# Optimization experiments

Hardware: AMD Instinct MI355X
Metric: run time of the kernel (lower is better)

## Reference

```python
import jax, jax.numpy as jnp
import numpy as np

DPITCH_RANGE = 24.0
SCALE = 1.0

B, T, ND, SD, H = 8192, 256, 8, 3, 64
HIST = 64
L = T - HIST  # generated LSTM steps; L+1 outputs emitted
IN = ND + SD + 1


def setup_inputs() -> dict:
    key = jax.random.key(0)
    ks = jax.random.split(key, 11)
    s = 1.0 / np.sqrt(H)

    def u(k, shape):
        return jax.random.uniform(k, shape, jnp.float32, -s, s)

    return {
        "noise": jax.random.normal(ks[0], (B, T, ND), jnp.float32),
        "hist_x": jax.random.normal(ks[1], (B, HIST, SD), jnp.float32) * 0.1,
        "gap_duration": jax.random.uniform(ks[2], (B, L + 1, SD - 1), jnp.float32),
        "W_ih": u(ks[3], (4 * H, IN)),
        "W_hh": u(ks[4], (4 * H, H)),
        "b_ih": u(ks[5], (4 * H,)),
        "b_hh": u(ks[6], (4 * H,)),
        "W1": u(ks[7], (H, H)),
        "b1": u(ks[8], (H,)),
        "W2": u(ks[9], (1, H)),
        "b2": u(ks[10], (1,)),
    }


def reference(noise, hist_x, gap_duration, W_ih, W_hh, b_ih, b_hh, W1, b1, W2, b2):
    hist_len = hist_x.shape[1]
    bias = b_ih + b_hh

    def lstm_cell(x, h, c):
        # PyTorch gate order: i, f, g, o
        gates = x @ W_ih.T + h @ W_hh.T + bias
        i, f, g, o = jnp.split(gates, 4, axis=-1)
        c = jax.nn.sigmoid(f) * c + jax.nn.sigmoid(i) * jnp.tanh(g)
        h = jax.nn.sigmoid(o) * jnp.tanh(c)
        return h, c

    # ---- conditioning on history ----
    dist = jnp.cumsum(hist_x[:, :, -1:], axis=1)                 # [B,HIST,1]
    cond_in = jnp.concatenate([hist_x, dist, noise[:, :hist_len]], axis=-1)  # [B,HIST,IN]
    h0 = jnp.zeros((noise.shape[0], W_hh.shape[1]), noise.dtype)
    c0 = jnp.zeros_like(h0)

    def cond_step(carry, x_t):
        h, c = carry
        h, c = lstm_cell(x_t, h, c)
        return (h, c), None

    (h, c), _ = jax.lax.scan(cond_step, (h0, c0), jnp.swapaxes(cond_in, 0, 1))
    output = h                      # last LSTM output [B,H]
    dist = dist[:, -1, :]           # [B,1]

    gen_noise = noise[:, hist_len:]                               # [B,L,ND]
    # pad one zero step: the final LSTM update is computed but unused
    gen_noise = jnp.concatenate(
        [gen_noise, jnp.zeros((gen_noise.shape[0], 1, gen_noise.shape[2]), gen_noise.dtype)], axis=1)
    xs = (jnp.swapaxes(gap_duration, 0, 1), jnp.swapaxes(gen_noise, 0, 1))

    def gen_step(carry, x_t):
        h, c, out, dist = carry
        gd, nz = x_t
        z = jnp.tanh(jnp.tanh(out @ W1.T + b1) @ W2.T + b2)       # output_net
        dp = z * DPITCH_RANGE * SCALE                             # [B,1]
        x = jnp.concatenate([gd, dp], axis=-1)                    # [B,SD]
        dist = dist + dp
        inp = jnp.concatenate([x, dist, nz], axis=-1)             # [B,IN]
        h, c = lstm_cell(inp, h, c)
        return (h, c, h, dist), x

    _, gen_xs = jax.lax.scan(gen_step, (h, c, output, dist), xs)  # [L+1,B,SD]
    output_seq = jnp.swapaxes(gen_xs, 0, 1)                       # [B,L+1,SD]
    return jnp.concatenate([hist_x, output_seq], axis=1)          # [B,HIST+L+1,SD]
```

## Files before the change

kernel.cpp:

```cpp
#include <hip/hip_runtime.h>
#include <stdint.h>

typedef unsigned short u16;
typedef unsigned int u32;
typedef __attribute__((ext_vector_type(8))) short short8v;
typedef __attribute__((ext_vector_type(4))) float f32x4;

#define NB 16
#define HISTN 64
#define TGEN 193

#define S_NOISE 2048
#define S_HIST  192
#define S_GAP   386
#define S_OUT   771

#define HROW 104

__device__ __forceinline__ float b2f(u16 u) { return __uint_as_float(((u32)u) << 16); }
__device__ __forceinline__ u16 f2b(float f) {
    u32 u = __float_as_uint(f);
    u32 r = (u + 0x7fffu + ((u >> 16) & 1u)) >> 16;
    return (u16)r;
}
__device__ __forceinline__ float rcp_(float x) { return __builtin_amdgcn_rcpf(x); }
__device__ __forceinline__ float sigf(float x) { return rcp_(1.0f + __expf(-x)); }
__device__ __forceinline__ float tanhf_(float x) {
    return __builtin_fmaf(-2.0f, rcp_(1.0f + __expf(2.0f * x)), 1.0f);
}
__device__ __forceinline__ float ldv(const void* p, int idx, bool f32) {
    return f32 ? ((const float*)p)[idx] : b2f(((const u16*)p)[idx]);
}
__device__ __forceinline__ void sync_lds() {
    asm volatile("s_waitcnt lgkmcnt(0)" ::: "memory");
    __builtin_amdgcn_s_barrier();
}

extern "C" __global__ void __launch_bounds__(512, 4)
lstm_gen_kernel(const void* __restrict__ noise, const void* __restrict__ hist_x,
                const void* __restrict__ gap, const void* __restrict__ pW_ih,
                const void* __restrict__ pW_hh, const void* __restrict__ pb_ih,
                const void* __restrict__ pb_hh, const void* __restrict__ pW1,
                const void* __restrict__ pb1, const void* __restrict__ pW2,
                const void* __restrict__ pb2, void* __restrict__ out)
{
    __shared__ u16 hst[NB * HROW];
    __shared__ float zpl[NB * 20];

    const int tid = threadIdx.x;
    const int lane = tid & 63;
    const int w = tid >> 6;
    const int lg = lane >> 4;
    const int ln = lane & 15;

    bool is_f32 = false;
    {
        const u32* p = (const u32*)pW_hh;
        for (int i = 0; i < 64; i++) {
            u32 v = p[i];
            float a = b2f((u16)(v & 0xffffu));
            float bb = b2f((u16)(v >> 16));
            if (!(fabsf(a) <= 0.5f) || !(fabsf(bb) <= 0.5f)) is_f32 = true;
        }
    }

    for (int i = tid; i < NB * HROW / 2; i += 512) ((u32*)hst)[i] = 0u;

    short8v a00, a01, a02, a10, a11, a12;
#pragma unroll
    for (int T = 0; T < 2; T++) {
        const int j = (T << 5) | (w << 2) | (ln >> 2);
        const int g = ln & 3;
        const int row = (g << 6) | j;
        float wdp = ldv(pW_ih, row * 12 + 2, is_f32);
        u16 wdph = f2b(wdp);
        u16 wdpl = f2b(wdp - b2f(wdph));
        float wds = ldv(pW_ih, row * 12 + 3, is_f32);
        u16 wdsh = f2b(wds);
        u16 wdsl = f2b(wds - b2f(wdsh));
        short8v f0, f1, f2;
#pragma unroll
        for (int e = 0; e < 8; e++) {
            const int c = lg * 8 + e;
            f0[e] = (short)f2b(ldv(pW_hh, row * 64 + c, is_f32));
            f1[e] = (short)f2b(ldv(pW_hh, row * 64 + 32 + c, is_f32));
            u16 v = 0;
            if (c == 0 || c == 1) v = f2b(ldv(pW_ih, row * 12 + c, is_f32));
            else if (c == 2 || c == 3) v = wdph;
            else if (c == 4 || c == 5) v = wdsh;
            else if (c == 6) v = wdsl;
            else if (c == 7) v = wdpl;
            else if (c >= 8 && c < 16) v = f2b(ldv(pW_ih, row * 12 + (c - 4), is_f32));
            f2[e] = (short)v;
        }
        if (T == 0) { a00 = f0; a01 = f1; a02 = f2; }
        else        { a10 = f0; a11 = f1; a12 = f2; }
    }

    f32x4 bias0, bias1;
#pragma unroll
    for (int T = 0; T < 2; T++) {
        const int jc = (T << 5) | (w << 2) | lg;
        f32x4 bv;
#pragma unroll
        for (int q = 0; q < 4; q++) {
            const int row = (q << 6) | jc;
            bv[q] = ldv(pb_ih, row, is_f32) + ldv(pb_hh, row, is_f32);
        }
        if (T == 0) bias0 = bv; else bias1 = bv;
    }

    const bool mlpw = (w >= 4);
    short8v w1F0 = {}, w1F1 = {};
    f32x4 b1v = {0.f, 0.f, 0.f, 0.f};
    float w2L[4] = {0.f, 0.f, 0.f, 0.f};
    if (mlpw) {
        const int wp = w - 4;
        const int row1 = (wp << 4) | ln;
#pragma unroll
        for (int e = 0; e < 8; e++) {
            w1F0[e] = (short)f2b(ldv(pW1, row1 * 64 + lg * 8 + e, is_f32));
            w1F1[e] = (short)f2b(ldv(pW1, row1 * 64 + 32 + lg * 8 + e, is_f32));
        }
        const int rq = (wp << 4) | (lg << 2);
#pragma unroll
        for (int q = 0; q < 4; q++) {
            b1v[q] = ldv(pb1, rq + q, is_f32);
            w2L[q] = ldv(pW2, rq + q, is_f32);
        }
    }

    const bool owner = tid < NB;
    const size_t gb = (size_t)blockIdx.x * NB + (size_t)(tid & (NB - 1));
    const u16* nz_h = (const u16*)noise + gb * S_NOISE;
    const float* nz_f = (const float*)noise + gb * S_NOISE;
    const u16* hx_h = (const u16*)hist_x + gb * S_HIST;
    const float* hx_f = (const float*)hist_x + gb * S_HIST;
    const u16* gd_h = (const u16*)gap + gb * S_GAP;
    const float* gd_f = (const float*)gap + gb * S_GAP;
    u16* out_h = (u16*)out + gb * S_OUT;
    float* out_f = (float*)out + gb * S_OUT;

    float dist = 0.0f, b2v = 0.0f;
    float cv0 = 0.f, cv1 = 0.f, cv2 = 0.f;
    u32 n01 = 0, n23 = 0, n45 = 0, n67 = 0;

    auto ldnoise = [&](int t) {
        if (is_f32) {
            const float4* q = (const float4*)(nz_f + t * 8);
            float4 a = q[0], bq = q[1];
            n01 = (u32)f2b(a.x) | ((u32)f2b(a.y) << 16);
            n23 = (u32)f2b(a.z) | ((u32)f2b(a.w) << 16);
            n45 = (u32)f2b(bq.x) | ((u32)f2b(bq.y) << 16);
            n67 = (u32)f2b(bq.z) | ((u32)f2b(bq.w) << 16);
        } else {
            uint4 nv = *(const uint4*)(nz_h + t * 8);
            n01 = nv.x; n23 = nv.y; n45 = nv.z; n67 = nv.w;
        }
    };

    if (owner) {
        b2v = ldv(pb2, 0, is_f32);
        if (is_f32) { cv0 = hx_f[0]; cv1 = hx_f[1]; cv2 = hx_f[2]; }
        else { cv0 = b2f(hx_h[0]); cv1 = b2f(hx_h[1]); cv2 = b2f(hx_h[2]); }
        ldnoise(0);
    }

    float cst0 = 0.f, cst1 = 0.f;
    __syncthreads();

#pragma unroll 1
    for (int t = 0; t < HISTN; t++) {
        short8v bf0 = *(const short8v*)&hst[ln * HROW + lg * 8];
        short8v bf1 = *(const short8v*)&hst[ln * HROW + 32 + lg * 8];
        if (owner) {
            dist += cv2;
            u16 dph = f2b(cv2); u16 dpl = f2b(cv2 - b2f(dph));
            u16 dsh = f2b(dist); u16 dsl = f2b(dist - b2f(dsh));
            u16* hr = &hst[tid * HROW];
            *(u32*)&hr[64] = (u32)f2b(cv0) | ((u32)f2b(cv1) << 16);
            *(u32*)&hr[66] = (u32)dph | ((u32)dpl << 16);
            *(u32*)&hr[68] = (u32)dsh | ((u32)dsl << 16);
            *(u32*)&hr[70] = (u32)dsh | ((u32)dph << 16);
            *(u32*)&hr[72] = n01; *(u32*)&hr[74] = n23;
            *(u32*)&hr[76] = n45; *(u32*)&hr[78] = n67;
        }
        sync_lds();
        if (owner) {
            if (is_f32) { out_f[t*3] = cv0; out_f[t*3+1] = cv1; out_f[t*3+2] = cv2; }
            else { out_h[t*3] = f2b(cv0); out_h[t*3+1] = f2b(cv1); out_h[t*3+2] = f2b(cv2); }
            if (t + 1 < HISTN) {
                if (is_f32) { cv0 = hx_f[(t+1)*3]; cv1 = hx_f[(t+1)*3+1]; cv2 = hx_f[(t+1)*3+2]; }
                else { cv0 = b2f(hx_h[(t+1)*3]); cv1 = b2f(hx_h[(t+1)*3+1]); cv2 = b2f(hx_h[(t+1)*3+2]); }
                ldnoise(t + 1);
            } else {
                if (is_f32) { cv0 = gd_f[0]; cv1 = gd_f[1]; }
                else { u32 g = *(const u32*)gd_h; cv0 = b2f((u16)(g & 0xffffu)); cv1 = b2f((u16)(g >> 16)); }
                ldnoise(HISTN);
            }
        }
        short8v bf2 = *(const short8v*)&hst[ln * HROW + 64 + lg * 8];
        f32x4 acc0 = bias0, acc1 = bias1;
        acc0 = __builtin_amdgcn_mfma_f32_16x16x32_bf16(a00, bf0, acc0, 0, 0, 0);
        acc0 = __builtin_amdgcn_mfma_f32_16x16x32_bf16(a01, bf1, acc0, 0, 0, 0);
        acc0 = __builtin_amdgcn_mfma_f32_16x16x32_bf16(a02, bf2, acc0, 0, 0, 0);
        acc1 = __builtin_amdgcn_mfma_f32_16x16x32_bf16(a10, bf0, acc1, 0, 0, 0);
        acc1 = __builtin_amdgcn_mfma_f32_16x16x32_bf16(a11, bf1, acc1, 0, 0, 0);
        acc1 = __builtin_amdgcn_mfma_f32_16x16x32_bf16(a12, bf2, acc1, 0, 0, 0);
        float h0, h1;
        { float iv = sigf(acc0[0]), fv = sigf(acc0[1]), gv = tanhf_(acc0[2]), ov = sigf(acc0[3]);
          cst0 = fv * cst0 + iv * gv; h0 = ov * tanhf_(cst0); }
        { float iv = sigf(acc1[0]), fv = sigf(acc1[1]), gv = tanhf_(acc1[2]), ov = sigf(acc1[3]);
          cst1 = fv * cst1 + iv * gv; h1 = ov * tanhf_(cst1); }
        const int j0 = (w << 2) | lg;
        hst[ln * HROW + j0] = f2b(h0);
        hst[ln * HROW + j0 + 32] = f2b(h1);
        sync_lds();
    }

#pragma unroll 1
    for (int tg = 0; tg < TGEN; tg++) {
        short8v bf0 = *(const short8v*)&hst[ln * HROW + lg * 8];
        short8v bf1 = *(const short8v*)&hst[ln * HROW + 32 + lg * 8];
        if (mlpw) {
            f32x4 m0 = b1v;
            m0 = __builtin_amdgcn_mfma_f32_16x16x32_bf16(w1F0, bf0, m0, 0, 0, 0);
            m0 = __builtin_amdgcn_mfma_f32_16x16x32_bf16(w1F1, bf1, m0, 0, 0, 0);
            float p0 = w2L[0] * tanhf_(m0[0]) + w2L[1] * tanhf_(m0[1])
                     + w2L[2] * tanhf_(m0[2]) + w2L[3] * tanhf_(m0[3]);
            zpl[ln * 20 + (((w - 4) << 2) | lg)] = p0;
        }
        sync_lds();
        if (owner) {
            const float4* zr = (const float4*)&zpl[tid * 20];
            float4 z0 = zr[0], z1 = zr[1], z2 = zr[2], z3 = zr[3];
            float pre2 = b2v + z0.x + z0.y + z0.z + z0.w + z1.x + z1.y + z1.z + z1.w
                       + z2.x + z2.y + z2.z + z2.w + z3.x + z3.y + z3.z + z3.w;
            float zz = tanhf_(pre2);
            float dp = 24.0f * zz;
            dist += dp;
            u16 dph = f2b(dp); u16 dpl = f2b(dp - b2f(dph));
            u16 dsh = f2b(dist); u16 dsl = f2b(dist - b2f(dsh));
            u16* hr = &hst[tid * HROW];
            *(u32*)&hr[64] = (u32)f2b(cv0) | ((u32)f2b(cv1) << 16);
            *(u32*)&hr[66] = (u32)dph | ((u32)dpl << 16);
            *(u32*)&hr[68] = (u32)dsh | ((u32)dsl << 16);
            *(u32*)&hr[70] = (u32)dsh | ((u32)dph << 16);
            *(u32*)&hr[72] = n01; *(u32*)&hr[74] = n23;
            *(u32*)&hr[76] = n45; *(u32*)&hr[78] = n67;
            const int to = HISTN + tg;
            if (is_f32) { out_f[to*3] = cv0; out_f[to*3+1] = cv1; out_f[to*3+2] = dp; }
            else { out_h[to*3] = f2b(cv0); out_h[to*3+1] = f2b(cv1); out_h[to*3+2] = f2b(dp); }
        }
        sync_lds();
        if (owner && tg + 1 < TGEN) {
            if (is_f32) { cv0 = gd_f[(tg+1)*2]; cv1 = gd_f[(tg+1)*2+1]; }
            else { u32 g = *(const u32*)(gd_h + (tg+1)*2);
                   cv0 = b2f((u16)(g & 0xffffu)); cv1 = b2f((u16)(g >> 16)); }
            if (tg + 1 < TGEN - 1) ldnoise(HISTN + tg + 1);
            else { n01 = n23 = n45 = n67 = 0; }
        }
        short8v bf2 = *(const short8v*)&hst[ln * HROW + 64 + lg * 8];
        f32x4 acc0 = bias0, acc1 = bias1;
        acc0 = __builtin_amdgcn_mfma_f32_16x16x32_bf16(a00, bf0, acc0, 0, 0, 0);
        acc0 = __builtin_amdgcn_mfma_f32_16x16x32_bf16(a01, bf1, acc0, 0, 0, 0);
        acc0 = __builtin_amdgcn_mfma_f32_16x16x32_bf16(a02, bf2, acc0, 0, 0, 0);
        acc1 = __builtin_amdgcn_mfma_f32_16x16x32_bf16(a10, bf0, acc1, 0, 0, 0);
        acc1 = __builtin_amdgcn_mfma_f32_16x16x32_bf16(a11, bf1, acc1, 0, 0, 0);
        acc1 = __builtin_amdgcn_mfma_f32_16x16x32_bf16(a12, bf2, acc1, 0, 0, 0);
        float h0, h1;
        { float iv = sigf(acc0[0]), fv = sigf(acc0[1]), gv = tanhf_(acc0[2]), ov = sigf(acc0[3]);
          cst0 = fv * cst0 + iv * gv; h0 = ov * tanhf_(cst0); }
        { float iv = sigf(acc1[0]), fv = sigf(acc1[1]), gv = tanhf_(acc1[2]), ov = sigf(acc1[3]);
          cst1 = fv * cst1 + iv * gv; h1 = ov * tanhf_(cst1); }
        const int j0 = (w << 2) | lg;
        hst[ln * HROW + j0] = f2b(h0);
        hst[ln * HROW + j0 + 32] = f2b(h1);
        sync_lds();
    }
}

extern "C" void kernel_launch(void* const* d_in, const int* in_sizes, int n_in,
                              void* d_out, int out_size, void* d_ws, size_t ws_size,
                              hipStream_t stream) {
    (void)in_sizes; (void)n_in; (void)d_ws; (void)ws_size; (void)out_size;
    lstm_gen_kernel<<<512, 512, 0, stream>>>(
        d_in[0], d_in[1], d_in[2], d_in[3], d_in[4], d_in[5],
        d_in[6], d_in[7], d_in[8], d_in[9], d_in[10], d_out);
}
```

Measured before the change: 500.6 us.

## Double-buffer hidden state and apply dist/dp terms in fp32 to cut barriers

```diff
diff --git a/kernel.cpp b/kernel.cpp
--- a/kernel.cpp
+++ b/kernel.cpp
@@ -44,8 +44,9 @@
                 const void* __restrict__ pb1, const void* __restrict__ pW2,
                 const void* __restrict__ pb2, void* __restrict__ out)
 {
-    __shared__ u16 hst[NB * HROW];
-    __shared__ float zpl[NB * 20];
+    __shared__ u16 hst[2][NB * HROW];
+    __shared__ float hxl[HISTN][NB][3];
+    __shared__ float zpl[NB * 4];
 
     const int tid = threadIdx.x;
     const int lane = tid & 63;
@@ -64,7 +65,11 @@
         }
     }
 
-    for (int i = tid; i < NB * HROW / 2; i += 512) ((u32*)hst)[i] = 0u;
+    for (int i = tid; i < NB * HROW; i += 512) ((u32*)hst)[i] = 0u;
+    for (int i = tid; i < HISTN * NB * 3; i += 512) {
+        int t = i / 48, r = i % 48, b = r / 3, k = r % 3;
+        hxl[t][b][k] = ldv(hist_x, ((size_t)blockIdx.x * NB + b) * S_HIST + t * 3 + k, is_f32);
+    }
 
     short8v a00, a01, a02, a10, a11, a12;
 #pragma unroll
@@ -72,12 +77,6 @@
         const int j = (T << 5) | (w << 2) | (ln >> 2);
         const int g = ln & 3;
         const int row = (g << 6) | j;
-        float wdp = ldv(pW_ih, row * 12 + 2, is_f32);
-        u16 wdph = f2b(wdp);
-        u16 wdpl = f2b(wdp - b2f(wdph));
-        float wds = ldv(pW_ih, row * 12 + 3, is_f32);
-        u16 wdsh = f2b(wds);
-        u16 wdsl = f2b(wds - b2f(wdsh));
         short8v f0, f1, f2;
 #pragma unroll
         for (int e = 0; e < 8; e++) {
@@ -86,10 +85,6 @@
             f1[e] = (short)f2b(ldv(pW_hh, row * 64 + 32 + c, is_f32));
             u16 v = 0;
             if (c == 0 || c == 1) v = f2b(ldv(pW_ih, row * 12 + c, is_f32));
-            else if (c == 2 || c == 3) v = wdph;
-            else if (c == 4 || c == 5) v = wdsh;
-            else if (c == 6) v = wdsl;
-            else if (c == 7) v = wdpl;
             else if (c >= 8 && c < 16) v = f2b(ldv(pW_ih, row * 12 + (c - 4), is_f32));
             f2[e] = (short)v;
         }
@@ -97,17 +92,20 @@
         else        { a10 = f0; a11 = f1; a12 = f2; }
     }
 
-    f32x4 bias0, bias1;
+    f32x4 bias0, bias1, wd0, wd1, ws0, ws1;
 #pragma unroll
     for (int T = 0; T < 2; T++) {
         const int jc = (T << 5) | (w << 2) | lg;
-        f32x4 bv;
+        f32x4 bv, dv, sv;
 #pragma unroll
         for (int q = 0; q < 4; q++) {
             const int row = (q << 6) | jc;
             bv[q] = ldv(pb_ih, row, is_f32) + ldv(pb_hh, row, is_f32);
-        }
-        if (T == 0) bias0 = bv; else bias1 = bv;
+            dv[q] = ldv(pW_ih, row * 12 + 2, is_f32);
+            sv[q] = ldv(pW_ih, row * 12 + 3, is_f32);
+        }
+        if (T == 0) { bias0 = bv; wd0 = dv; ws0 = sv; }
+        else        { bias1 = bv; wd1 = dv; ws1 = sv; }
     }
 
     const bool mlpw = (w >= 4);
@@ -130,19 +128,19 @@
         }
     }
 
-    const bool owner = tid < NB;
-    const size_t gb = (size_t)blockIdx.x * NB + (size_t)(tid & (NB - 1));
+    const float b2v = ldv(pb2, 0, is_f32);
+
+    const size_t gb = (size_t)blockIdx.x * NB + (size_t)ln;
     const u16* nz_h = (const u16*)noise + gb * S_NOISE;
     const float* nz_f = (const float*)noise + gb * S_NOISE;
-    const u16* hx_h = (const u16*)hist_x + gb * S_HIST;
-    const float* hx_f = (const float*)hist_x + gb * S_HIST;
     const u16* gd_h = (const u16*)gap + gb * S_GAP;
     const float* gd_f = (const float*)gap + gb * S_GAP;
     u16* out_h = (u16*)out + gb * S_OUT;
     float* out_f = (float*)out + gb * S_OUT;
-
-    float dist = 0.0f, b2v = 0.0f;
-    float cv0 = 0.f, cv1 = 0.f, cv2 = 0.f;
+    const bool writer = (tid < NB);
+
+    float dist = 0.0f;
+    float cv0 = 0.f, cv1 = 0.f;
     u32 n01 = 0, n23 = 0, n45 = 0, n67 = 0;
 
     auto ldnoise = [&](int t) {
@@ -158,48 +156,39 @@
             n01 = nv.x; n23 = nv.y; n45 = nv.z; n67 = nv.w;
         }
     };
-
-    if (owner) {
-        b2v = ldv(pb2, 0, is_f32);
-        if (is_f32) { cv0 = hx_f[0]; cv1 = hx_f[1]; cv2 = hx_f[2]; }
-        else { cv0 = b2f(hx_h[0]); cv1 = b2f(hx_h[1]); cv2 = b2f(hx_h[2]); }
-        ldnoise(0);
-    }
-
+    auto ldgd = [&](int tg) {
+        if (is_f32) { cv0 = gd_f[tg * 2]; cv1 = gd_f[tg * 2 + 1]; }
+        else { u32 g = *(const u32*)(gd_h + tg * 2);
+               cv0 = b2f((u16)(g & 0xffffu)); cv1 = b2f((u16)(g >> 16)); }
+    };
+    auto mkbf2 = [&](float xa, float xb) {
+        short8v z = {};
+        if (lg == 0) { z[0] = (short)f2b(xa); z[1] = (short)f2b(xb); }
+        else if (lg == 1) {
+            z[0] = (short)(n01 & 0xffffu); z[1] = (short)(n01 >> 16);
+            z[2] = (short)(n23 & 0xffffu); z[3] = (short)(n23 >> 16);
+            z[4] = (short)(n45 & 0xffffu); z[5] = (short)(n45 >> 16);
+            z[6] = (short)(n67 & 0xffffu); z[7] = (short)(n67 >> 16);
+        }
+        return z;
+    };
+
+    if (lg == 1) ldnoise(0);
     float cst0 = 0.f, cst1 = 0.f;
+    int pc = 0;
     __syncthreads();
 
 #pragma unroll 1
     for (int t = 0; t < HISTN; t++) {
-        short8v bf0 = *(const short8v*)&hst[ln * HROW + lg * 8];
-        short8v bf1 = *(const short8v*)&hst[ln * HROW + 32 + lg * 8];
-        if (owner) {
-            dist += cv2;
-            u16 dph = f2b(cv2); u16 dpl = f2b(cv2 - b2f(dph));
-            u16 dsh = f2b(dist); u16 dsl = f2b(dist - b2f(dsh));
-            u16* hr = &hst[tid * HROW];
-            *(u32*)&hr[64] = (u32)f2b(cv0) | ((u32)f2b(cv1) << 16);
-            *(u32*)&hr[66] = (u32)dph | ((u32)dpl << 16);
-            *(u32*)&hr[68] = (u32)dsh | ((u32)dsl << 16);
-            *(u32*)&hr[70] = (u32)dsh | ((u32)dph << 16);
-            *(u32*)&hr[72] = n01; *(u32*)&hr[74] = n23;
-            *(u32*)&hr[76] = n45; *(u32*)&hr[78] = n67;
-        }
-        sync_lds();
-        if (owner) {
-            if (is_f32) { out_f[t*3] = cv0; out_f[t*3+1] = cv1; out_f[t*3+2] = cv2; }
-            else { out_h[t*3] = f2b(cv0); out_h[t*3+1] = f2b(cv1); out_h[t*3+2] = f2b(cv2); }
-            if (t + 1 < HISTN) {
-                if (is_f32) { cv0 = hx_f[(t+1)*3]; cv1 = hx_f[(t+1)*3+1]; cv2 = hx_f[(t+1)*3+2]; }
-                else { cv0 = b2f(hx_h[(t+1)*3]); cv1 = b2f(hx_h[(t+1)*3+1]); cv2 = b2f(hx_h[(t+1)*3+2]); }
-                ldnoise(t + 1);
-            } else {
-                if (is_f32) { cv0 = gd_f[0]; cv1 = gd_f[1]; }
-                else { u32 g = *(const u32*)gd_h; cv0 = b2f((u16)(g & 0xffffu)); cv1 = b2f((u16)(g >> 16)); }
-                ldnoise(HISTN);
-            }
-        }
-        short8v bf2 = *(const short8v*)&hst[ln * HROW + 64 + lg * 8];
+        const u16* hc = hst[pc];
+        u16* hn = hst[pc ^ 1];
+        short8v bf0 = *(const short8v*)&hc[ln * HROW + lg * 8];
+        short8v bf1 = *(const short8v*)&hc[ln * HROW + 32 + lg * 8];
+        float x2 = hxl[t][ln][2];
+        float x0f = 0.f, x1f = 0.f;
+        if (lg == 0) { x0f = hxl[t][ln][0]; x1f = hxl[t][ln][1]; }
+        dist += x2;
+        short8v bf2 = mkbf2(x0f, x1f);
         f32x4 acc0 = bias0, acc1 = bias1;
         acc0 = __builtin_amdgcn_mfma_f32_16x16x32_bf16(a00, bf0, acc0, 0, 0, 0);
         acc0 = __builtin_amdgcn_mfma_f32_16x16x32_bf16(a01, bf1, acc0, 0, 0, 0);
@@ -207,60 +196,36 @@
         acc1 = __builtin_amdgcn_mfma_f32_16x16x32_bf16(a10, bf0, acc1, 0, 0, 0);
         acc1 = __builtin_amdgcn_mfma_f32_16x16x32_bf16(a11, bf1, acc1, 0, 0, 0);
         acc1 = __builtin_amdgcn_mfma_f32_16x16x32_bf16(a12, bf2, acc1, 0, 0, 0);
+#pragma unroll
+        for (int q = 0; q < 4; q++) {
+            acc0[q] += wd0[q] * x2 + ws0[q] * dist;
+            acc1[q] += wd1[q] * x2 + ws1[q] * dist;
+        }
         float h0, h1;
         { float iv = sigf(acc0[0]), fv = sigf(acc0[1]), gv = tanhf_(acc0[2]), ov = sigf(acc0[3]);
           cst0 = fv * cst0 + iv * gv; h0 = ov * tanhf_(cst0); }
         { float iv = sigf(acc1[0]), fv = sigf(acc1[1]), gv = tanhf_(acc1[2]), ov = sigf(acc1[3]);
           cst1 = fv * cst1 + iv * gv; h1 = ov * tanhf_(cst1); }
         const int j0 = (w << 2) | lg;
-        hst[ln * HROW + j0] = f2b(h0);
-        hst[ln * HROW + j0 + 32] = f2b(h1);
+        hn[ln * HROW + j0] = f2b(h0);
+        hn[ln * HROW + j0 + 32] = f2b(h1);
+        if (writer) {
+            if (is_f32) { out_f[t*3] = x0f; out_f[t*3+1] = x1f; out_f[t*3+2] = x2; }
+            else { out_h[t*3] = f2b(x0f); out_h[t*3+1] = f2b(x1f); out_h[t*3+2] = f2b(x2); }
+        }
+        if (lg == 1) ldnoise(t + 1 < HISTN ? t + 1 : HISTN);
+        if (lg == 0 && t == HISTN - 1) ldgd(0);
         sync_lds();
+        pc ^= 1;
     }
 
 #pragma unroll 1
     for (int tg = 0; tg < TGEN; tg++) {
-        short8v bf0 = *(const short8v*)&hst[ln * HROW + lg * 8];
-        short8v bf1 = *(const short8v*)&hst[ln * HROW + 32 + lg * 8];
-        if (mlpw) {
-            f32x4 m0 = b1v;
-            m0 = __builtin_amdgcn_mfma_f32_16x16x32_bf16(w1F0, bf0, m0, 0, 0, 0);
-            m0 = __builtin_amdgcn_mfma_f32_16x16x32_bf16(w1F1, bf1, m0, 0, 0, 0);
-            float p0 = w2L[0] * tanhf_(m0[0]) + w2L[1] * tanhf_(m0[1])
-                     + w2L[2] * tanhf_(m0[2]) + w2L[3] * tanhf_(m0[3]);
-            zpl[ln * 20 + (((w - 4) << 2) | lg)] = p0;
-        }
-        sync_lds();
-        if (owner) {
-            const float4* zr = (const float4*)&zpl[tid * 20];
-            float4 z0 = zr[0], z1 = zr[1], z2 = zr[2], z3 = zr[3];
-            float pre2 = b2v + z0.x + z0.y + z0.z + z0.w + z1.x + z1.y + z1.z + z1.w
-                       + z2.x + z2.y + z2.z + z2.w + z3.x + z3.y + z3.z + z3.w;
-            float zz = tanhf_(pre2);
-            float dp = 24.0f * zz;
-            dist += dp;
-            u16 dph = f2b(dp); u16 dpl = f2b(dp - b2f(dph));
-            u16 dsh = f2b(dist); u16 dsl = f2b(dist - b2f(dsh));
-            u16* hr = &hst[tid * HROW];
-            *(u32*)&hr[64] = (u32)f2b(cv0) | ((u32)f2b(cv1) << 16);
-            *(u32*)&hr[66] = (u32)dph | ((u32)dpl << 16);
-            *(u32*)&hr[68] = (u32)dsh | ((u32)dsl << 16);
-            *(u32*)&hr[70] = (u32)dsh | ((u32)dph << 16);
-            *(u32*)&hr[72] = n01; *(u32*)&hr[74] = n23;
-            *(u32*)&hr[76] = n45; *(u32*)&hr[78] = n67;
-            const int to = HISTN + tg;
-            if (is_f32) { out_f[to*3] = cv0; out_f[to*3+1] = cv1; out_f[to*3+2] = dp; }
-            else { out_h[to*3] = f2b(cv0); out_h[to*3+1] = f2b(cv1); out_h[to*3+2] = f2b(dp); }
-        }
-        sync_lds();
-        if (owner && tg + 1 < TGEN) {
-            if (is_f32) { cv0 = gd_f[(tg+1)*2]; cv1 = gd_f[(tg+1)*2+1]; }
-            else { u32 g = *(const u32*)(gd_h + (tg+1)*2);
-                   cv0 = b2f((u16)(g & 0xffffu)); cv1 = b2f((u16)(g >> 16)); }
-            if (tg + 1 < TGEN - 1) ldnoise(HISTN + tg + 1);
-            else { n01 = n23 = n45 = n67 = 0; }
-        }
-        short8v bf2 = *(const short8v*)&hst[ln * HROW + 64 + lg * 8];
+        const u16* hc = hst[pc];
+        u16* hn = hst[pc ^ 1];
+        short8v bf0 = *(const short8v*)&hc[ln * HROW + lg * 8];
+        short8v bf1 = *(const short8v*)&hc[ln * HROW + 32 + lg * 8];
+        short8v bf2 = mkbf2(cv0, cv1);
         f32x4 acc0 = bias0, acc1 = bias1;
         acc0 = __builtin_amdgcn_mfma_f32_16x16x32_bf16(a00, bf0, acc0, 0, 0, 0);
         acc0 = __builtin_amdgcn_mfma_f32_16x16x32_bf16(a01, bf1, acc0, 0, 0, 0);
@@ -268,15 +233,47 @@
         acc1 = __builtin_amdgcn_mfma_f32_16x16x32_bf16(a10, bf0, acc1, 0, 0, 0);
         acc1 = __builtin_amdgcn_mfma_f32_16x16x32_bf16(a11, bf1, acc1, 0, 0, 0);
         acc1 = __builtin_amdgcn_mfma_f32_16x16x32_bf16(a12, bf2, acc1, 0, 0, 0);
+        if (mlpw) {
+            f32x4 m0 = b1v;
+            m0 = __builtin_amdgcn_mfma_f32_16x16x32_bf16(w1F0, bf0, m0, 0, 0, 0);
+            m0 = __builtin_amdgcn_mfma_f32_16x16x32_bf16(w1F1, bf1, m0, 0, 0, 0);
+            float p = w2L[0] * tanhf_(m0[0]) + w2L[1] * tanhf_(m0[1])
+                    + w2L[2] * tanhf_(m0[2]) + w2L[3] * tanhf_(m0[3]);
+            p += __shfl_xor(p, 16);
+            p += __shfl_xor(p, 32);
+            if (lg == 0) zpl[(ln << 2) | (w - 4)] = p;
+        }
+        sync_lds();
+        float4 zr = *(const float4*)&zpl[ln << 2];
+        float dp = 24.0f * tanhf_(b2v + zr.x + zr.y + zr.z + zr.w);
+        dist += dp;
+#pragma unroll
+        for (int q = 0; q < 4; q++) {
+            acc0[q] += wd0[q] * dp + ws0[q] * dist;
+            acc1[q] += wd1[q] * dp + ws1[q] * dist;
+        }
         float h0, h1;
         { float iv = sigf(acc0[0]), fv = sigf(acc0[1]), gv = tanhf_(acc0[2]), ov = sigf(acc0[3]);
           cst0 = fv * cst0 + iv * gv; h0 = ov * tanhf_(cst0); }
         { float iv = sigf(acc1[0]), fv = sigf(acc1[1]), gv = tanhf_(acc1[2]), ov = sigf(acc1[3]);
           cst1 = fv * cst1 + iv * gv; h1 = ov * tanhf_(cst1); }
         const int j0 = (w << 2) | lg;
-        hst[ln * HROW + j0] = f2b(h0);
-        hst[ln * HROW + j0 + 32] = f2b(h1);
+        hn[ln * HROW + j0] = f2b(h0);
+        hn[ln * HROW + j0 + 32] = f2b(h1);
+        if (writer) {
+            const int to = HISTN + tg;
+            if (is_f32) { out_f[to*3] = cv0; out_f[to*3+1] = cv1; out_f[to*3+2] = dp; }
+            else { out_h[to*3] = f2b(cv0); out_h[to*3+1] = f2b(cv1); out_h[to*3+2] = f2b(dp); }
+        }
+        if (tg + 1 < TGEN) {
+            if (lg == 0) ldgd(tg + 1);
+            if (lg == 1) {
+                if (tg + 1 < TGEN - 1) ldnoise(HISTN + tg + 1);
+                else { n01 = n23 = n45 = n67 = 0; }
+            }
+        }
         sync_lds();
+        pc ^= 1;
     }
 }
 
```

Result: slower. 580.5 us (+16.0%).

## Split LSTM gate work across 16 waves, one hidden-unit tile per wave

Applied to the files above, without the earlier changes.

```diff
diff --git a/kernel.cpp b/kernel.cpp
--- a/kernel.cpp
+++ b/kernel.cpp
@@ -36,7 +36,7 @@
     __builtin_amdgcn_s_barrier();
 }
 
-extern "C" __global__ void __launch_bounds__(512, 4)
+extern "C" __global__ void __launch_bounds__(1024, 8)
 lstm_gen_kernel(const void* __restrict__ noise, const void* __restrict__ hist_x,
                 const void* __restrict__ gap, const void* __restrict__ pW_ih,
                 const void* __restrict__ pW_hh, const void* __restrict__ pb_ih,
@@ -64,12 +64,11 @@
         }
     }
 
-    for (int i = tid; i < NB * HROW / 2; i += 512) ((u32*)hst)[i] = 0u;
-
-    short8v a00, a01, a02, a10, a11, a12;
-#pragma unroll
-    for (int T = 0; T < 2; T++) {
-        const int j = (T << 5) | (w << 2) | (ln >> 2);
+    for (int i = tid; i < NB * HROW / 2; i += 1024) ((u32*)hst)[i] = 0u;
+
+    short8v a0, a1, a2;
+    {
+        const int j = (w << 2) | (ln >> 2);
         const int g = ln & 3;
         const int row = (g << 6) | j;
         float wdp = ldv(pW_ih, row * 12 + 2, is_f32);
@@ -78,12 +77,11 @@
         float wds = ldv(pW_ih, row * 12 + 3, is_f32);
         u16 wdsh = f2b(wds);
         u16 wdsl = f2b(wds - b2f(wdsh));
-        short8v f0, f1, f2;
 #pragma unroll
         for (int e = 0; e < 8; e++) {
             const int c = lg * 8 + e;
-            f0[e] = (short)f2b(ldv(pW_hh, row * 64 + c, is_f32));
-            f1[e] = (short)f2b(ldv(pW_hh, row * 64 + 32 + c, is_f32));
+            a0[e] = (short)f2b(ldv(pW_hh, row * 64 + c, is_f32));
+            a1[e] = (short)f2b(ldv(pW_hh, row * 64 + 32 + c, is_f32));
             u16 v = 0;
             if (c == 0 || c == 1) v = f2b(ldv(pW_ih, row * 12 + c, is_f32));
             else if (c == 2 || c == 3) v = wdph;
@@ -91,31 +89,26 @@
             else if (c == 6) v = wdsl;
             else if (c == 7) v = wdpl;
             else if (c >= 8 && c < 16) v = f2b(ldv(pW_ih, row * 12 + (c - 4), is_f32));
-            f2[e] = (short)v;
-        }
-        if (T == 0) { a00 = f0; a01 = f1; a02 = f2; }
-        else        { a10 = f0; a11 = f1; a12 = f2; }
-    }
-
-    f32x4 bias0, bias1;
-#pragma unroll
-    for (int T = 0; T < 2; T++) {
-        const int jc = (T << 5) | (w << 2) | lg;
-        f32x4 bv;
+            a2[e] = (short)v;
+        }
+    }
+
+    f32x4 bias0;
+    {
+        const int jc = (w << 2) | lg;
 #pragma unroll
         for (int q = 0; q < 4; q++) {
             const int row = (q << 6) | jc;
-            bv[q] = ldv(pb_ih, row, is_f32) + ldv(pb_hh, row, is_f32);
-        }
-        if (T == 0) bias0 = bv; else bias1 = bv;
-    }
-
-    const bool mlpw = (w >= 4);
+            bias0[q] = ldv(pb_ih, row, is_f32) + ldv(pb_hh, row, is_f32);
+        }
+    }
+
+    const bool mlpw = (w >= 12);
     short8v w1F0 = {}, w1F1 = {};
     f32x4 b1v = {0.f, 0.f, 0.f, 0.f};
     float w2L[4] = {0.f, 0.f, 0.f, 0.f};
     if (mlpw) {
-        const int wp = w - 4;
+        const int wp = w - 12;
         const int row1 = (wp << 4) | ln;
 #pragma unroll
         for (int e = 0; e < 8; e++) {
@@ -166,7 +159,7 @@
         ldnoise(0);
     }
 
-    float cst0 = 0.f, cst1 = 0.f;
+    float cst0 = 0.f;
     __syncthreads();
 
 #pragma unroll 1
@@ -200,21 +193,14 @@
             }
         }
         short8v bf2 = *(const short8v*)&hst[ln * HROW + 64 + lg * 8];
-        f32x4 acc0 = bias0, acc1 = bias1;
-        acc0 = __builtin_amdgcn_mfma_f32_16x16x32_bf16(a00, bf0, acc0, 0, 0, 0);
-        acc0 = __builtin_amdgcn_mfma_f32_16x16x32_bf16(a01, bf1, acc0, 0, 0, 0);
-        acc0 = __builtin_amdgcn_mfma_f32_16x16x32_bf16(a02, bf2, acc0, 0, 0, 0);
-        acc1 = __builtin_amdgcn_mfma_f32_16x16x32_bf16(a10, bf0, acc1, 0, 0, 0);
-        acc1 = __builtin_amdgcn_mfma_f32_16x16x32_bf16(a11, bf1, acc1, 0, 0, 0);
-        acc1 = __builtin_amdgcn_mfma_f32_16x16x32_bf16(a12, bf2, acc1, 0, 0, 0);
-        float h0, h1;
+        f32x4 acc0 = bias0;
+        acc0 = __builtin_amdgcn_mfma_f32_16x16x32_bf16(a0, bf0, acc0, 0, 0, 0);
+        acc0 = __builtin_amdgcn_mfma_f32_16x16x32_bf16(a1, bf1, acc0, 0, 0, 0);
+        acc0 = __builtin_amdgcn_mfma_f32_16x16x32_bf16(a2, bf2, acc0, 0, 0, 0);
+        float h0;
         { float iv = sigf(acc0[0]), fv = sigf(acc0[1]), gv = tanhf_(acc0[2]), ov = sigf(acc0[3]);
           cst0 = fv * cst0 + iv * gv; h0 = ov * tanhf_(cst0); }
-        { float iv = sigf(acc1[0]), fv = sigf(acc1[1]), gv = tanhf_(acc1[2]), ov = sigf(acc1[3]);
-          cst1 = fv * cst1 + iv * gv; h1 = ov * tanhf_(cst1); }
-        const int j0 = (w << 2) | lg;
-        hst[ln * HROW + j0] = f2b(h0);
-        hst[ln * HROW + j0 + 32] = f2b(h1);
+        hst[ln * HROW + ((w << 2) | lg)] = f2b(h0);
         sync_lds();
     }
 
@@ -228,7 +214,7 @@
             m0 = __builtin_amdgcn_mfma_f32_16x16x32_bf16(w1F1, bf1, m0, 0, 0, 0);
             float p0 = w2L[0] * tanhf_(m0[0]) + w2L[1] * tanhf_(m0[1])
                      + w2L[2] * tanhf_(m0[2]) + w2L[3] * tanhf_(m0[3]);
-            zpl[ln * 20 + (((w - 4) << 2) | lg)] = p0;
+            zpl[ln * 20 + (((w - 12) << 2) | lg)] = p0;
         }
         sync_lds();
         if (owner) {
@@ -261,21 +247,14 @@
             else { n01 = n23 = n45 = n67 = 0; }
         }
         short8v bf2 = *(const short8v*)&hst[ln * HROW + 64 + lg * 8];
-        f32x4 acc0 = bias0, acc1 = bias1;
-        acc0 = __builtin_amdgcn_mfma_f32_16x16x32_bf16(a00, bf0, acc0, 0, 0, 0);
-        acc0 = __builtin_amdgcn_mfma_f32_16x16x32_bf16(a01, bf1, acc0, 0, 0, 0);
-        acc0 = __builtin_amdgcn_mfma_f32_16x16x32_bf16(a02, bf2, acc0, 0, 0, 0);
-        acc1 = __builtin_amdgcn_mfma_f32_16x16x32_bf16(a10, bf0, acc1, 0, 0, 0);
-        acc1 = __builtin_amdgcn_mfma_f32_16x16x32_bf16(a11, bf1, acc1, 0, 0, 0);
-        acc1 = __builtin_amdgcn_mfma_f32_16x16x32_bf16(a12, bf2, acc1, 0, 0, 0);
-        float h0, h1;
+        f32x4 acc0 = bias0;
+        acc0 = __builtin_amdgcn_mfma_f32_16x16x32_bf16(a0, bf0, acc0, 0, 0, 0);
+        acc0 = __builtin_amdgcn_mfma_f32_16x16x32_bf16(a1, bf1, acc0, 0, 0, 0);
+        acc0 = __builtin_amdgcn_mfma_f32_16x16x32_bf16(a2, bf2, acc0, 0, 0, 0);
+        float h0;
         { float iv = sigf(acc0[0]), fv = sigf(acc0[1]), gv = tanhf_(acc0[2]), ov = sigf(acc0[3]);
           cst0 = fv * cst0 + iv * gv; h0 = ov * tanhf_(cst0); }
-        { float iv = sigf(acc1[0]), fv = sigf(acc1[1]), gv = tanhf_(acc1[2]), ov = sigf(acc1[3]);
-          cst1 = fv * cst1 + iv * gv; h1 = ov * tanhf_(cst1); }
-        const int j0 = (w << 2) | lg;
-        hst[ln * HROW + j0] = f2b(h0);
-        hst[ln * HROW + j0 + 32] = f2b(h1);
+        hst[ln * HROW + ((w << 2) | lg)] = f2b(h0);
         sync_lds();
     }
 }
@@ -284,7 +263,7 @@
                               void* d_out, int out_size, void* d_ws, size_t ws_size,
                               hipStream_t stream) {
     (void)in_sizes; (void)n_in; (void)d_ws; (void)ws_size; (void)out_size;
-    lstm_gen_kernel<<<512, 512, 0, stream>>>(
+    lstm_gen_kernel<<<512, 1024, 0, stream>>>(
         d_in[0], d_in[1], d_in[2], d_in[3], d_in[4], d_in[5],
         d_in[6], d_in[7], d_in[8], d_in[9], d_in[10], d_out);
 }
```

Measured after the change: 740.5 us. +47.9%, slower.

## Restructure generation step to cut barriers and apply dp/dist terms in fp32

Applied to the files above, without the earlier changes.

```diff
diff --git a/kernel.cpp b/kernel.cpp
--- a/kernel.cpp
+++ b/kernel.cpp
@@ -45,7 +45,10 @@
                 const void* __restrict__ pb2, void* __restrict__ out)
 {
     __shared__ u16 hst[NB * HROW];
-    __shared__ float zpl[NB * 20];
+    __shared__ float zpl[NB * 4];
+    __shared__ float gds[TGEN][NB][2];
+    __shared__ u16 nring[32][NB][8];
+    __shared__ float dpd[NB];
 
     const int tid = threadIdx.x;
     const int lane = tid & 63;
@@ -65,6 +68,10 @@
     }
 
     for (int i = tid; i < NB * HROW / 2; i += 512) ((u32*)hst)[i] = 0u;
+    for (int i = tid; i < TGEN * NB * 2; i += 512) {
+        int t = i >> 5, r = i & 31, b = r >> 1, k = r & 1;
+        gds[t][b][k] = ldv(gap, ((size_t)blockIdx.x * NB + b) * S_GAP + t * 2 + k, is_f32);
+    }
 
     short8v a00, a01, a02, a10, a11, a12;
 #pragma unroll
@@ -97,17 +104,20 @@
         else        { a10 = f0; a11 = f1; a12 = f2; }
     }
 
-    f32x4 bias0, bias1;
+    f32x4 bias0, bias1, wd0, wd1, ws0, ws1;
 #pragma unroll
     for (int T = 0; T < 2; T++) {
         const int jc = (T << 5) | (w << 2) | lg;
-        f32x4 bv;
+        f32x4 bv, dv, sv;
 #pragma unroll
         for (int q = 0; q < 4; q++) {
             const int row = (q << 6) | jc;
             bv[q] = ldv(pb_ih, row, is_f32) + ldv(pb_hh, row, is_f32);
-        }
-        if (T == 0) bias0 = bv; else bias1 = bv;
+            dv[q] = ldv(pW_ih, row * 12 + 2, is_f32);
+            sv[q] = ldv(pW_ih, row * 12 + 3, is_f32);
+        }
+        if (T == 0) { bias0 = bv; wd0 = dv; ws0 = sv; }
+        else        { bias1 = bv; wd1 = dv; ws1 = sv; }
     }
 
     const bool mlpw = (w >= 4);
@@ -130,18 +140,18 @@
         }
     }
 
+    const float b2v = ldv(pb2, 0, is_f32);
+
     const bool owner = tid < NB;
     const size_t gb = (size_t)blockIdx.x * NB + (size_t)(tid & (NB - 1));
     const u16* nz_h = (const u16*)noise + gb * S_NOISE;
     const float* nz_f = (const float*)noise + gb * S_NOISE;
     const u16* hx_h = (const u16*)hist_x + gb * S_HIST;
     const float* hx_f = (const float*)hist_x + gb * S_HIST;
-    const u16* gd_h = (const u16*)gap + gb * S_GAP;
-    const float* gd_f = (const float*)gap + gb * S_GAP;
     u16* out_h = (u16*)out + gb * S_OUT;
     float* out_f = (float*)out + gb * S_OUT;
 
-    float dist = 0.0f, b2v = 0.0f;
+    float dist = 0.0f;
     float cv0 = 0.f, cv1 = 0.f, cv2 = 0.f;
     u32 n01 = 0, n23 = 0, n45 = 0, n67 = 0;
 
@@ -160,7 +170,6 @@
     };
 
     if (owner) {
-        b2v = ldv(pb2, 0, is_f32);
         if (is_f32) { cv0 = hx_f[0]; cv1 = hx_f[1]; cv2 = hx_f[2]; }
         else { cv0 = b2f(hx_h[0]); cv1 = b2f(hx_h[1]); cv2 = b2f(hx_h[2]); }
         ldnoise(0);
@@ -193,10 +202,6 @@
                 if (is_f32) { cv0 = hx_f[(t+1)*3]; cv1 = hx_f[(t+1)*3+1]; cv2 = hx_f[(t+1)*3+2]; }
                 else { cv0 = b2f(hx_h[(t+1)*3]); cv1 = b2f(hx_h[(t+1)*3+1]); cv2 = b2f(hx_h[(t+1)*3+2]); }
                 ldnoise(t + 1);
-            } else {
-                if (is_f32) { cv0 = gd_f[0]; cv1 = gd_f[1]; }
-                else { u32 g = *(const u32*)gd_h; cv0 = b2f((u16)(g & 0xffffu)); cv1 = b2f((u16)(g >> 16)); }
-                ldnoise(HISTN);
             }
         }
         short8v bf2 = *(const short8v*)&hst[ln * HROW + 64 + lg * 8];
@@ -218,49 +223,40 @@
         sync_lds();
     }
 
+    if (owner) dpd[tid] = dist;
+    {
+        const int s = tid >> 4, b = tid & 15;
+        const int t = HISTN + s;
+        u32 r0, r1, r2, r3;
+        if (is_f32) {
+            const float* nf = (const float*)noise + ((size_t)blockIdx.x * NB + b) * S_NOISE + t * 8;
+            float4 a = *(const float4*)nf, bq = *(const float4*)(nf + 4);
+            r0 = (u32)f2b(a.x) | ((u32)f2b(a.y) << 16);
+            r1 = (u32)f2b(a.z) | ((u32)f2b(a.w) << 16);
+            r2 = (u32)f2b(bq.x) | ((u32)f2b(bq.y) << 16);
+            r3 = (u32)f2b(bq.z) | ((u32)f2b(bq.w) << 16);
+        } else {
+            uint4 nv = *(const uint4*)((const u16*)noise + ((size_t)blockIdx.x * NB + b) * S_NOISE + t * 8);
+            r0 = nv.x; r1 = nv.y; r2 = nv.z; r3 = nv.w;
+        }
+        u32* dst = (u32*)&nring[s][b][0];
+        dst[0] = r0; dst[1] = r1; dst[2] = r2; dst[3] = r3;
+    }
+    sync_lds();
+    dist = dpd[ln];
+
 #pragma unroll 1
     for (int tg = 0; tg < TGEN; tg++) {
         short8v bf0 = *(const short8v*)&hst[ln * HROW + lg * 8];
         short8v bf1 = *(const short8v*)&hst[ln * HROW + 32 + lg * 8];
-        if (mlpw) {
-            f32x4 m0 = b1v;
-            m0 = __builtin_amdgcn_mfma_f32_16x16x32_bf16(w1F0, bf0, m0, 0, 0, 0);
-            m0 = __builtin_amdgcn_mfma_f32_16x16x32_bf16(w1F1, bf1, m0, 0, 0, 0);
-            float p0 = w2L[0] * tanhf_(m0[0]) + w2L[1] * tanhf_(m0[1])
-                     + w2L[2] * tanhf_(m0[2]) + w2L[3] * tanhf_(m0[3]);
-            zpl[ln * 20 + (((w - 4) << 2) | lg)] = p0;
-        }
-        sync_lds();
-        if (owner) {
-            const float4* zr = (const float4*)&zpl[tid * 20];
-            float4 z0 = zr[0], z1 = zr[1], z2 = zr[2], z3 = zr[3];
-            float pre2 = b2v + z0.x + z0.y + z0.z + z0.w + z1.x + z1.y + z1.z + z1.w
-                       + z2.x + z2.y + z2.z + z2.w + z3.x + z3.y + z3.z + z3.w;
-            float zz = tanhf_(pre2);
-            float dp = 24.0f * zz;
-            dist += dp;
-            u16 dph = f2b(dp); u16 dpl = f2b(dp - b2f(dph));
-            u16 dsh = f2b(dist); u16 dsl = f2b(dist - b2f(dsh));
-            u16* hr = &hst[tid * HROW];
-            *(u32*)&hr[64] = (u32)f2b(cv0) | ((u32)f2b(cv1) << 16);
-            *(u32*)&hr[66] = (u32)dph | ((u32)dpl << 16);
-            *(u32*)&hr[68] = (u32)dsh | ((u32)dsl << 16);
-            *(u32*)&hr[70] = (u32)dsh | ((u32)dph << 16);
-            *(u32*)&hr[72] = n01; *(u32*)&hr[74] = n23;
-            *(u32*)&hr[76] = n45; *(u32*)&hr[78] = n67;
-            const int to = HISTN + tg;
-            if (is_f32) { out_f[to*3] = cv0; out_f[to*3+1] = cv1; out_f[to*3+2] = dp; }
-            else { out_h[to*3] = f2b(cv0); out_h[to*3+1] = f2b(cv1); out_h[to*3+2] = f2b(dp); }
-        }
-        sync_lds();
-        if (owner && tg + 1 < TGEN) {
-            if (is_f32) { cv0 = gd_f[(tg+1)*2]; cv1 = gd_f[(tg+1)*2+1]; }
-            else { u32 g = *(const u32*)(gd_h + (tg+1)*2);
-                   cv0 = b2f((u16)(g & 0xffffu)); cv1 = b2f((u16)(g >> 16)); }
-            if (tg + 1 < TGEN - 1) ldnoise(HISTN + tg + 1);
-            else { n01 = n23 = n45 = n67 = 0; }
-        }
-        short8v bf2 = *(const short8v*)&hst[ln * HROW + 64 + lg * 8];
+        float2 g2 = *(const float2*)&gds[tg][ln][0];
+        short8v bf2 = {};
+        if (lg == 0) { bf2[0] = (short)f2b(g2.x); bf2[1] = (short)f2b(g2.y); }
+        else if (lg == 1) {
+            union { uint4 u; short8v s; } cvt;
+            cvt.u = *(const uint4*)&nring[tg & 31][ln][0];
+            bf2 = cvt.s;
+        }
         f32x4 acc0 = bias0, acc1 = bias1;
         acc0 = __builtin_amdgcn_mfma_f32_16x16x32_bf16(a00, bf0, acc0, 0, 0, 0);
         acc0 = __builtin_amdgcn_mfma_f32_16x16x32_bf16(a01, bf1, acc0, 0, 0, 0);
@@ -268,6 +264,45 @@
         acc1 = __builtin_amdgcn_mfma_f32_16x16x32_bf16(a10, bf0, acc1, 0, 0, 0);
         acc1 = __builtin_amdgcn_mfma_f32_16x16x32_bf16(a11, bf1, acc1, 0, 0, 0);
         acc1 = __builtin_amdgcn_mfma_f32_16x16x32_bf16(a12, bf2, acc1, 0, 0, 0);
+        if (mlpw) {
+            f32x4 m0 = b1v;
+            m0 = __builtin_amdgcn_mfma_f32_16x16x32_bf16(w1F0, bf0, m0, 0, 0, 0);
+            m0 = __builtin_amdgcn_mfma_f32_16x16x32_bf16(w1F1, bf1, m0, 0, 0, 0);
+            float p = w2L[0] * tanhf_(m0[0]) + w2L[1] * tanhf_(m0[1])
+                    + w2L[2] * tanhf_(m0[2]) + w2L[3] * tanhf_(m0[3]);
+            p += __shfl_xor(p, 16);
+            p += __shfl_xor(p, 32);
+            if (lg == 0) zpl[(ln << 2) | (w - 4)] = p;
+        }
+        if (((tg & 15) == 0) && tg > 0 && tg <= 176 && tid < 256) {
+            const int s = tid >> 4, b = tid & 15;
+            const int t = HISTN + tg + 16 + s;
+            u32 r0 = 0, r1 = 0, r2 = 0, r3 = 0;
+            if (t < 256) {
+                if (is_f32) {
+                    const float* nf = (const float*)noise + ((size_t)blockIdx.x * NB + b) * S_NOISE + t * 8;
+                    float4 a = *(const float4*)nf, bq = *(const float4*)(nf + 4);
+                    r0 = (u32)f2b(a.x) | ((u32)f2b(a.y) << 16);
+                    r1 = (u32)f2b(a.z) | ((u32)f2b(a.w) << 16);
+                    r2 = (u32)f2b(bq.x) | ((u32)f2b(bq.y) << 16);
+                    r3 = (u32)f2b(bq.z) | ((u32)f2b(bq.w) << 16);
+                } else {
+                    uint4 nv = *(const uint4*)((const u16*)noise + ((size_t)blockIdx.x * NB + b) * S_NOISE + t * 8);
+                    r0 = nv.x; r1 = nv.y; r2 = nv.z; r3 = nv.w;
+                }
+            }
+            u32* dst = (u32*)&nring[(tg + 16 + s) & 31][b][0];
+            dst[0] = r0; dst[1] = r1; dst[2] = r2; dst[3] = r3;
+        }
+        sync_lds();
+        f32x4 zr = *(const f32x4*)&zpl[ln << 2];
+        float dp = 24.0f * tanhf_(b2v + zr[0] + zr[1] + zr[2] + zr[3]);
+        dist += dp;
+#pragma unroll
+        for (int q = 0; q < 4; q++) {
+            acc0[q] += wd0[q] * dp + ws0[q] * dist;
+            acc1[q] += wd1[q] * dp + ws1[q] * dist;
+        }
         float h0, h1;
         { float iv = sigf(acc0[0]), fv = sigf(acc0[1]), gv = tanhf_(acc0[2]), ov = sigf(acc0[3]);
           cst0 = fv * cst0 + iv * gv; h0 = ov * tanhf_(cst0); }
@@ -276,6 +311,11 @@
         const int j0 = (w << 2) | lg;
         hst[ln * HROW + j0] = f2b(h0);
         hst[ln * HROW + j0 + 32] = f2b(h1);
+        if (tid < NB) {
+            const int to = HISTN + tg;
+            if (is_f32) { out_f[to*3] = g2.x; out_f[to*3+1] = g2.y; out_f[to*3+2] = dp; }
+            else { out_h[to*3] = f2b(g2.x); out_h[to*3+1] = f2b(g2.y); out_h[to*3+2] = f2b(dp); }
+        }
         sync_lds();
     }
 }
```

Measured after the change: 479.2 us. 4.3% less time.
